# Kernel optimization log

Measured on AMD Instinct MI355X. Metric: run time of the kernel, lower is better.

## Reference

```python
import jax, jax.numpy as jnp
import numpy as np

N_NODES = 100000
N_EDGES = 3200000
IN_DIM = 512
OUT_DIM = 256


def setup_inputs() -> dict:
    key = jax.random.key(0)
    k1, k2, k3, k4, k5 = jax.random.split(key, 5)
    features = jax.random.normal(k1, (N_NODES, IN_DIM), dtype=jnp.float32)
    adj_rows = jax.random.randint(k2, (N_EDGES,), 0, N_NODES, dtype=jnp.int32)
    adj_cols = jax.random.randint(k3, (N_EDGES,), 0, N_NODES, dtype=jnp.int32)
    # normalized adjacency values (e.g., 1/sqrt(d_i d_j)); random positive here
    adj_vals = jax.random.uniform(k4, (N_EDGES,), dtype=jnp.float32) * (1.0 / 32.0)
    # xavier uniform for kernel
    limit = np.sqrt(6.0 / (IN_DIM + OUT_DIM)).astype(np.float32)
    kernel = jax.random.uniform(k5, (IN_DIM, OUT_DIM), dtype=jnp.float32, minval=-limit, maxval=limit)
    bias = jnp.zeros((OUT_DIM,), dtype=jnp.float32)
    skip_weight = jnp.ones((OUT_DIM,), dtype=jnp.float32)
    return {
        "features": features,
        "adj_rows": adj_rows,
        "adj_cols": adj_cols,
        "adj_vals": adj_vals,
        "kernel": kernel,
        "bias": bias,
        "skip_weight": skip_weight,
    }


def reference(features, adj_rows, adj_cols, adj_vals, kernel, bias, skip_weight):
    # dense feature transform: [N, in] @ [in, out] -> [N, out]
    xw = jnp.matmul(features, kernel)
    # SpMM: aggregate[i] = sum_e val[e] * xw[col[e]] over edges with row[e] == i
    msgs = adj_vals[:, None] * xw[adj_cols]            # [E, out] gather
    agg = jax.ops.segment_sum(msgs, adj_rows, num_segments=N_NODES)  # [N, out] scatter-add
    out = xw * skip_weight + agg + bias                # skip scale + bias epilogue
    return jax.nn.selu(out)
```

## Files before the change

### kernel.cpp

```cpp
#include <hip/hip_runtime.h>
#include <hip/hip_bf16.h>
#include <cstdint>
#include <cstddef>

#define IN_DIM 512
#define OUT_DIM 256
#define BROWS 128
#define NBUCK_MAX 1024
#define CAP 4608

typedef __bf16 bf16x8 __attribute__((ext_vector_type(8)));
typedef float f32x4 __attribute__((ext_vector_type(4)));

__device__ __forceinline__ unsigned short f2bf(float f) {
    __bf16 h = (__bf16)f;
    return __builtin_bit_cast(unsigned short, h);
}
__device__ __forceinline__ float bf2f(unsigned short u) {
    unsigned int x = ((unsigned int)u) << 16;
    return __builtin_bit_cast(float, x);
}
__device__ __forceinline__ float selu(float x) {
    const float kScale = 1.0507009873554805f;
    const float kAlpha = 1.6732632423543772f;
    return (x > 0.f) ? kScale * x : kScale * kAlpha * (expf(x) - 1.f);
}

__global__ void k_convW(const float* __restrict__ W, unsigned short* __restrict__ Wt) {
    int idx = blockIdx.x * 256 + threadIdx.x;
    int n = idx & (OUT_DIM - 1);
    int k = idx >> 8;
    if (k < IN_DIM) Wt[n * IN_DIM + k] = f2bf(W[k * OUT_DIM + n]);
}

__launch_bounds__(512, 2)
__global__ void k_gemm(const float* __restrict__ A, const unsigned short* __restrict__ Wt,
                       signed char* __restrict__ xq, float* __restrict__ scales, int M) {
    __shared__ unsigned short lA[128 * 32];
    __shared__ unsigned short lB[256 * 32];
    __shared__ float lrm[128];
    const int t = threadIdx.x;
    const int wave = t >> 6, lane = t & 63;
    const int wr = wave >> 2, wc = wave & 3;
    const int m0 = blockIdx.x * 128;
    const int mlo = lane & 15, kq = lane >> 4;

    if (t < 128) lrm[t] = 0.f;

    f32x4 acc[4][4] = {};

    for (int k0 = 0; k0 < IN_DIM; k0 += 32) {
        #pragma unroll
        for (int p = 0; p < 2; ++p) {
            int idx = p * 512 + t;
            int r = idx >> 3, c4 = idx & 7;
            int gr = m0 + r; if (gr >= M) gr = M - 1;
            const float4 v = *reinterpret_cast<const float4*>(&A[(size_t)gr * IN_DIM + k0 + c4 * 4]);
            ushort4 u;
            u.x = f2bf(v.x); u.y = f2bf(v.y); u.z = f2bf(v.z); u.w = f2bf(v.w);
            *reinterpret_cast<ushort4*>(&lA[r * 32 + c4 * 4]) = u;
        }
        #pragma unroll
        for (int p = 0; p < 2; ++p) {
            int idx = p * 512 + t;
            int n = idx >> 2, c8 = idx & 3;
            const uint4 v = *reinterpret_cast<const uint4*>(&Wt[(size_t)n * IN_DIM + k0 + c8 * 8]);
            *reinterpret_cast<uint4*>(&lB[n * 32 + c8 * 8]) = v;
        }
        __syncthreads();

        bf16x8 af[4], bfr[4];
        #pragma unroll
        for (int mt = 0; mt < 4; ++mt)
            af[mt] = *reinterpret_cast<const bf16x8*>(&lA[(wr * 64 + mt * 16 + mlo) * 32 + kq * 8]);
        #pragma unroll
        for (int nt = 0; nt < 4; ++nt)
            bfr[nt] = *reinterpret_cast<const bf16x8*>(&lB[(wc * 64 + nt * 16 + mlo) * 32 + kq * 8]);
        #pragma unroll
        for (int mt = 0; mt < 4; ++mt)
            #pragma unroll
            for (int nt = 0; nt < 4; ++nt)
                acc[mt][nt] = __builtin_amdgcn_mfma_f32_16x16x32_bf16(af[mt], bfr[nt], acc[mt][nt], 0, 0, 0);
        __syncthreads();
    }

    #pragma unroll
    for (int mt = 0; mt < 4; ++mt) {
        #pragma unroll
        for (int i = 0; i < 4; ++i) {
            float m = fmaxf(fmaxf(fabsf(acc[mt][0][i]), fabsf(acc[mt][1][i])),
                            fmaxf(fabsf(acc[mt][2][i]), fabsf(acc[mt][3][i])));
            m = fmaxf(m, __shfl_xor(m, 1));
            m = fmaxf(m, __shfl_xor(m, 2));
            m = fmaxf(m, __shfl_xor(m, 4));
            m = fmaxf(m, __shfl_xor(m, 8));
            if (mlo == 0)
                atomicMax(reinterpret_cast<int*>(&lrm[wr * 64 + mt * 16 + kq * 4 + i]),
                          __float_as_int(m));
        }
    }
    __syncthreads();

    #pragma unroll
    for (int mt = 0; mt < 4; ++mt) {
        #pragma unroll
        for (int i = 0; i < 4; ++i) {
            const int rl = wr * 64 + mt * 16 + kq * 4 + i;
            const int row = m0 + rl;
            const float rm = lrm[rl];
            const float inv = (rm > 0.f) ? (127.f / rm) : 0.f;
            if (row < M) {
                #pragma unroll
                for (int nt = 0; nt < 4; ++nt) {
                    int q = (int)rintf(acc[mt][nt][i] * inv);
                    xq[(size_t)row * OUT_DIM + wc * 64 + nt * 16 + mlo] = (signed char)q;
                }
            }
        }
    }
    if (t < 128) {
        int row = m0 + t;
        if (row < M) scales[row] = lrm[t] * (1.f / 127.f);
    }
}

__launch_bounds__(512)
__global__ void k_bhist(const int* __restrict__ rows, int* __restrict__ bcnt, int E) {
    __shared__ int cnt[NBUCK_MAX];
    const int t = threadIdx.x;
    const int base = blockIdx.x * 8192;
    cnt[t] = 0; cnt[t + 512] = 0;
    __syncthreads();
    #pragma unroll
    for (int p = 0; p < 4; ++p) {
        const int i = base + p * 2048 + (t << 2);
        if (i + 4 <= E) {
            int4 r4 = *reinterpret_cast<const int4*>(&rows[i]);
            atomicAdd(&cnt[r4.x >> 7], 1);
            atomicAdd(&cnt[r4.y >> 7], 1);
            atomicAdd(&cnt[r4.z >> 7], 1);
            atomicAdd(&cnt[r4.w >> 7], 1);
        } else if (i < E) {
            for (int j = i; j < E && j < i + 4; ++j) atomicAdd(&cnt[rows[j] >> 7], 1);
        }
    }
    __syncthreads();
    if (cnt[t] > 0) atomicAdd(&bcnt[t], cnt[t]);
    if (cnt[t + 512] > 0) atomicAdd(&bcnt[t + 512], cnt[t + 512]);
}

__launch_bounds__(NBUCK_MAX)
__global__ void k_bscan(const int* __restrict__ bcnt, int* __restrict__ bbase,
                        int* __restrict__ bcursor, int nbuck, int E) {
    const int t = threadIdx.x;
    __shared__ int sh[NBUCK_MAX];
    int v = (t < nbuck) ? bcnt[t] : 0;
    sh[t] = v;
    __syncthreads();
    for (int off = 1; off < NBUCK_MAX; off <<= 1) {
        int x = (t >= off) ? sh[t - off] : 0;
        __syncthreads();
        sh[t] += x;
        __syncthreads();
    }
    int ex = sh[t] - v;
    bbase[t] = ex;
    bcursor[t] = ex;
    if (t == 0) bbase[NBUCK_MAX] = E;
}

__launch_bounds__(512)
__global__ void k_bin(const int* __restrict__ rows, const int* __restrict__ cols,
                      const float* __restrict__ vals, const float* __restrict__ scales,
                      int* __restrict__ bcursor, int2* __restrict__ binned, int E) {
    __shared__ int cnt[NBUCK_MAX];
    __shared__ int scn[512];
    __shared__ int dlt[NBUCK_MAX];
    const int t = threadIdx.x;
    const int base = blockIdx.x * 8192;

    cnt[t] = 0; cnt[t + 512] = 0;
    __syncthreads();

    int er[16], ec[16];
    float ev[16];
    #pragma unroll
    for (int p = 0; p < 4; ++p) {
        const int i = base + p * 2048 + (t << 2);
        if (i + 4 <= E) {
            int4 r4 = *reinterpret_cast<const int4*>(&rows[i]);
            int4 c4 = *reinterpret_cast<const int4*>(&cols[i]);
            float4 v4 = *reinterpret_cast<const float4*>(&vals[i]);
            er[4*p+0] = r4.x; ec[4*p+0] = c4.x; ev[4*p+0] = v4.x * scales[c4.x];
            er[4*p+1] = r4.y; ec[4*p+1] = c4.y; ev[4*p+1] = v4.y * scales[c4.y];
            er[4*p+2] = r4.z; ec[4*p+2] = c4.z; ev[4*p+2] = v4.z * scales[c4.z];
            er[4*p+3] = r4.w; ec[4*p+3] = c4.w; ev[4*p+3] = v4.w * scales[c4.w];
        } else {
            #pragma unroll
            for (int j = 0; j < 4; ++j) {
                int idx = i + j;
                bool ok = idx < E;
                er[4*p+j] = ok ? rows[idx] : -1;
                ec[4*p+j] = ok ? cols[idx] : 0;
                ev[4*p+j] = ok ? vals[idx] * scales[cols[idx]] : 0.f;
            }
        }
    }

    #pragma unroll
    for (int k = 0; k < 16; ++k)
        if (er[k] >= 0) atomicAdd(&cnt[er[k] >> 7], 1);
    __syncthreads();

    int v0 = cnt[2 * t], v1 = cnt[2 * t + 1];
    int s = v0 + v1;
    scn[t] = s;
    __syncthreads();
    for (int off = 1; off < 512; off <<= 1) {
        int x = (t >= off) ? scn[t - off] : 0;
        __syncthreads();
        scn[t] += x;
        __syncthreads();
    }
    int exp_ = scn[t] - s;
    int ex0 = exp_, ex1 = exp_ + v0;

    int d0 = 0, d1 = 0;
    if (v0 > 0) d0 = atomicAdd(&bcursor[2 * t], v0) - ex0;
    if (v1 > 0) d1 = atomicAdd(&bcursor[2 * t + 1], v1) - ex1;
    dlt[2 * t] = d0; dlt[2 * t + 1] = d1;
    cnt[2 * t] = ex0; cnt[2 * t + 1] = ex1;
    __syncthreads();

    #pragma unroll
    for (int k = 0; k < 16; ++k) {
        if (er[k] >= 0) {
            int b = er[k] >> 7;
            int lp = atomicAdd(&cnt[b], 1);
            binned[(size_t)(dlt[b] + lp)] =
                make_int2(ec[k] | ((er[k] & 127) << 17), __float_as_int(ev[k]));
        }
    }
}

__launch_bounds__(512)
__global__ void k_aggb(const signed char* __restrict__ xq,
                       const float* __restrict__ scales,
                       const int2* __restrict__ binned,
                       const int* __restrict__ bbase,
                       const float* __restrict__ skipw,
                       const float* __restrict__ bias,
                       float* __restrict__ out, int M) {
    __shared__ int2 lrec[CAP];
    __shared__ int lrs[BROWS + 1];
    __shared__ int lcur[BROWS];
    const int b = blockIdx.x, t = threadIdx.x;
    const int wave = t >> 6, lane = t & 63;
    const int start = bbase[b], end = bbase[b + 1];
    const int cnt = end - start;
    const int d4 = lane * 4;

    if (cnt <= CAP) {
        if (t < BROWS) lcur[t] = 0;
        __syncthreads();
        for (int i = start + t; i < end; i += 512)
            atomicAdd(&lcur[binned[i].x >> 17], 1);
        __syncthreads();
        int v = 0;
        if (t < BROWS) { v = lcur[t]; lrs[t] = v; }
        __syncthreads();
        for (int off = 1; off < BROWS; off <<= 1) {
            int x = 0;
            if (t < BROWS && t >= off) x = lrs[t - off];
            __syncthreads();
            if (t < BROWS) lrs[t] += x;
            __syncthreads();
        }
        int ex = 0;
        if (t < BROWS) ex = lrs[t] - v;
        __syncthreads();
        if (t < BROWS) { lrs[t] = ex; lcur[t] = ex; }
        if (t == 0) lrs[BROWS] = cnt;
        __syncthreads();
        for (int i = start + t; i < end; i += 512) {
            int2 rec = binned[i];
            int pos = atomicAdd(&lcur[rec.x >> 17], 1);
            lrec[pos] = rec;
        }
        __syncthreads();
        for (int rr = 0; rr < BROWS / 8; ++rr) {
            const int r = wave * (BROWS / 8) + rr;
            const int grow = b * BROWS + r;
            if (grow >= M) continue;
            const int s = lrs[r], e = lrs[r + 1];
            float a0 = 0.f, a1 = 0.f, a2 = 0.f, a3 = 0.f;
            int p = s;
            for (; p + 8 <= e; p += 8) {
                int cs[8]; float vs[8];
                #pragma unroll
                for (int u = 0; u < 8; ++u) {
                    int2 c = lrec[p + u];
                    cs[u] = c.x & 0x1FFFF; vs[u] = __int_as_float(c.y);
                }
                int g[8];
                #pragma unroll
                for (int u = 0; u < 8; ++u)
                    g[u] = *reinterpret_cast<const int*>(&xq[(size_t)cs[u] * OUT_DIM + d4]);
                #pragma unroll
                for (int u = 0; u < 8; ++u) {
                    a0 += vs[u] * (float)(signed char)(g[u]);
                    a1 += vs[u] * (float)(signed char)(g[u] >> 8);
                    a2 += vs[u] * (float)(signed char)(g[u] >> 16);
                    a3 += vs[u] * (float)(g[u] >> 24);
                }
            }
            for (; p < e; ++p) {
                int2 c = lrec[p];
                float v2 = __int_as_float(c.y);
                int g = *reinterpret_cast<const int*>(&xq[(size_t)(c.x & 0x1FFFF) * OUT_DIM + d4]);
                a0 += v2 * (float)(signed char)(g);
                a1 += v2 * (float)(signed char)(g >> 8);
                a2 += v2 * (float)(signed char)(g >> 16);
                a3 += v2 * (float)(g >> 24);
            }
            int w = *reinterpret_cast<const int*>(&xq[(size_t)grow * OUT_DIM + d4]);
            float sc = scales[grow];
            float x0 = (float)(signed char)(w)        * sc;
            float x1 = (float)(signed char)(w >> 8)   * sc;
            float x2 = (float)(signed char)(w >> 16)  * sc;
            float x3 = (float)(w >> 24)               * sc;
            float4 sw = *reinterpret_cast<const float4*>(&skipw[d4]);
            float4 bi = *reinterpret_cast<const float4*>(&bias[d4]);
            float4 r4;
            r4.x = selu(a0 + x0 * sw.x + bi.x);
            r4.y = selu(a1 + x1 * sw.y + bi.y);
            r4.z = selu(a2 + x2 * sw.z + bi.z);
            r4.w = selu(a3 + x3 * sw.w + bi.w);
            *reinterpret_cast<float4*>(&out[(size_t)grow * OUT_DIM + d4]) = r4;
        }
    } else {
        for (int rr = 0; rr < BROWS / 8; ++rr) {
            const int r = wave * (BROWS / 8) + rr;
            const int grow = b * BROWS + r;
            if (grow >= M) continue;
            float a0 = 0.f, a1 = 0.f, a2 = 0.f, a3 = 0.f;
            for (int i = start; i < end; ++i) {
                int2 c = binned[i];
                if ((c.x >> 17) != r) continue;
                float v2 = __int_as_float(c.y);
                int g = *reinterpret_cast<const int*>(&xq[(size_t)(c.x & 0x1FFFF) * OUT_DIM + d4]);
                a0 += v2 * (float)(signed char)(g);
                a1 += v2 * (float)(signed char)(g >> 8);
                a2 += v2 * (float)(signed char)(g >> 16);
                a3 += v2 * (float)(g >> 24);
            }
            int w = *reinterpret_cast<const int*>(&xq[(size_t)grow * OUT_DIM + d4]);
            float sc = scales[grow];
            float x0 = (float)(signed char)(w)        * sc;
            float x1 = (float)(signed char)(w >> 8)   * sc;
            float x2 = (float)(signed char)(w >> 16)  * sc;
            float x3 = (float)(w >> 24)               * sc;
            float4 sw = *reinterpret_cast<const float4*>(&skipw[d4]);
            float4 bi = *reinterpret_cast<const float4*>(&bias[d4]);
            float4 r4;
            r4.x = selu(a0 + x0 * sw.x + bi.x);
            r4.y = selu(a1 + x1 * sw.y + bi.y);
            r4.z = selu(a2 + x2 * sw.z + bi.z);
            r4.w = selu(a3 + x3 * sw.w + bi.w);
            *reinterpret_cast<float4*>(&out[(size_t)grow * OUT_DIM + d4]) = r4;
        }
    }
}

__global__ void k_hist(const int* __restrict__ rows, int* __restrict__ counts, int E) {
    int i = (blockIdx.x * 256 + threadIdx.x) * 4;
    if (i + 4 <= E) {
        int4 r = *reinterpret_cast<const int4*>(&rows[i]);
        atomicAdd(&counts[r.x], 1);
        atomicAdd(&counts[r.y], 1);
        atomicAdd(&counts[r.z], 1);
        atomicAdd(&counts[r.w], 1);
    } else {
        for (int j = i; j < E; ++j) atomicAdd(&counts[rows[j]], 1);
    }
}

__global__ void k_scan1(const int* __restrict__ counts, int* __restrict__ rs,
                        int* __restrict__ bsum, int N) {
    int b = blockIdx.x, t = threadIdx.x;
    int base = b * 1024 + t * 4;
    int4 v = make_int4(0, 0, 0, 0);
    if (base + 4 <= N) v = *reinterpret_cast<const int4*>(&counts[base]);
    else {
        if (base + 0 < N) v.x = counts[base + 0];
        if (base + 1 < N) v.y = counts[base + 1];
        if (base + 2 < N) v.z = counts[base + 2];
        if (base + 3 < N) v.w = counts[base + 3];
    }
    int s0 = v.x, s1 = s0 + v.y, s2 = s1 + v.z, s3 = s2 + v.w;
    __shared__ int sh[256];
    sh[t] = s3; __syncthreads();
    for (int off = 1; off < 256; off <<= 1) {
        int x = (t >= off) ? sh[t - off] : 0;
        __syncthreads();
        sh[t] += x;
        __syncthreads();
    }
    int ex = sh[t] - s3;
    if (base + 0 < N) rs[base + 0] = ex;
    if (base + 1 < N) rs[base + 1] = ex + s0;
    if (base + 2 < N) rs[base + 2] = ex + s1;
    if (base + 3 < N) rs[base + 3] = ex + s2;
    if (t == 255) bsum[b] = sh[255];
}

__global__ void k_scan2(const int* __restrict__ bsum, int* __restrict__ boff, int nb) {
    int t = threadIdx.x;
    __shared__ int sh[256];
    int v = (t < nb) ? bsum[t] : 0;
    sh[t] = v; __syncthreads();
    for (int off = 1; off < 256; off <<= 1) {
        int x = (t >= off) ? sh[t - off] : 0;
        __syncthreads();
        sh[t] += x;
        __syncthreads();
    }
    if (t < nb) boff[t] = sh[t] - v;
}

__global__ void k_scan3(int* __restrict__ rs, int* __restrict__ cursor,
                        const int* __restrict__ boff, int N, int E) {
    int b = blockIdx.x, t = threadIdx.x;
    int base = b * 1024 + t * 4;
    int o = boff[b];
    #pragma unroll
    for (int j = 0; j < 4; ++j) {
        if (base + j < N) {
            int v = rs[base + j] + o;
            rs[base + j] = v;
            cursor[base + j] = v;
        }
    }
    if (b == 0 && t == 0) rs[N] = E;
}

__global__ void k_scatter(const int* __restrict__ rows, const int* __restrict__ cols,
                          const float* __restrict__ vals, const float* __restrict__ scales,
                          int* __restrict__ cursor, int2* __restrict__ ecv, int E) {
    int i = (blockIdx.x * 256 + threadIdx.x) * 4;
    if (i + 4 <= E) {
        int4 r = *reinterpret_cast<const int4*>(&rows[i]);
        int4 c = *reinterpret_cast<const int4*>(&cols[i]);
        float4 v = *reinterpret_cast<const float4*>(&vals[i]);
        int p0 = atomicAdd(&cursor[r.x], 1); ecv[p0] = make_int2(c.x, __float_as_int(v.x * scales[c.x]));
        int p1 = atomicAdd(&cursor[r.y], 1); ecv[p1] = make_int2(c.y, __float_as_int(v.y * scales[c.y]));
        int p2 = atomicAdd(&cursor[r.z], 1); ecv[p2] = make_int2(c.z, __float_as_int(v.z * scales[c.z]));
        int p3 = atomicAdd(&cursor[r.w], 1); ecv[p3] = make_int2(c.w, __float_as_int(v.w * scales[c.w]));
    } else {
        for (int j = i; j < E; ++j) {
            int p = atomicAdd(&cursor[rows[j]], 1);
            ecv[p] = make_int2(cols[j], __float_as_int(vals[j] * scales[cols[j]]));
        }
    }
}

__launch_bounds__(256)
__global__ void k_agg(const signed char* __restrict__ xq,
                      const float* __restrict__ scales,
                      const int2* __restrict__ ecv,
                      const int* __restrict__ rs,
                      const float* __restrict__ skipw,
                      const float* __restrict__ bias,
                      float* __restrict__ out, int M) {
    const int wave = threadIdx.x >> 6, lane = threadIdx.x & 63;
    const int node = blockIdx.x * 4 + wave;
    if (node >= M) return;
    const int s = __builtin_amdgcn_readfirstlane(rs[node]);
    const int e = __builtin_amdgcn_readfirstlane(rs[node + 1]);
    const int d4 = lane * 4;

    float a0 = 0.f, a1 = 0.f, a2 = 0.f, a3 = 0.f;
    int p = s;
    constexpr int U = 8;
    for (; p + U <= e; p += U) {
        int   cs[U];
        float vs[U];
        #pragma unroll
        for (int u = 0; u < U; ++u) {
            int2 c = ecv[p + u];
            cs[u] = c.x; vs[u] = __int_as_float(c.y);
        }
        int g[U];
        #pragma unroll
        for (int u = 0; u < U; ++u)
            g[u] = *reinterpret_cast<const int*>(&xq[(size_t)cs[u] * OUT_DIM + d4]);
        #pragma unroll
        for (int u = 0; u < U; ++u) {
            a0 += vs[u] * (float)(signed char)(g[u]);
            a1 += vs[u] * (float)(signed char)(g[u] >> 8);
            a2 += vs[u] * (float)(signed char)(g[u] >> 16);
            a3 += vs[u] * (float)(g[u] >> 24);
        }
    }
    for (; p < e; ++p) {
        int2 c = ecv[p];
        float v = __int_as_float(c.y);
        int g = *reinterpret_cast<const int*>(&xq[(size_t)c.x * OUT_DIM + d4]);
        a0 += v * (float)(signed char)(g);
        a1 += v * (float)(signed char)(g >> 8);
        a2 += v * (float)(signed char)(g >> 16);
        a3 += v * (float)(g >> 24);
    }

    int w = *reinterpret_cast<const int*>(&xq[(size_t)node * OUT_DIM + d4]);
    float sc = scales[node];
    float x0 = (float)(signed char)(w)        * sc;
    float x1 = (float)(signed char)(w >> 8)   * sc;
    float x2 = (float)(signed char)(w >> 16)  * sc;
    float x3 = (float)(w >> 24)               * sc;

    float4 sw = *reinterpret_cast<const float4*>(&skipw[d4]);
    float4 bi = *reinterpret_cast<const float4*>(&bias[d4]);
    float4 r;
    r.x = selu(a0 + x0 * sw.x + bi.x);
    r.y = selu(a1 + x1 * sw.y + bi.y);
    r.z = selu(a2 + x2 * sw.z + bi.z);
    r.w = selu(a3 + x3 * sw.w + bi.w);
    *reinterpret_cast<float4*>(&out[(size_t)node * OUT_DIM + d4]) = r;
}

extern "C" void kernel_launch(void* const* d_in, const int* in_sizes, int n_in,
                              void* d_out, int out_size, void* d_ws, size_t ws_size,
                              hipStream_t stream) {
    const float* features = (const float*)d_in[0];
    const int*   adj_rows = (const int*)d_in[1];
    const int*   adj_cols = (const int*)d_in[2];
    const float* adj_vals = (const float*)d_in[3];
    const float* Wk       = (const float*)d_in[4];
    const float* bias     = (const float*)d_in[5];
    const float* skipw    = (const float*)d_in[6];
    float* out = (float*)d_out;

    const int M = in_sizes[0] / IN_DIM;
    const int E = in_sizes[1];

    char* w = (char*)d_ws;
    size_t off = 0;
    auto carve = [&](size_t bytes) -> void* {
        void* p = w + off;
        off = (off + bytes + 255) & ~(size_t)255;
        return p;
    };
    signed char* xq = (signed char*)carve((size_t)M * OUT_DIM);
    float* scales   = (float*)carve((size_t)M * 4);
    unsigned short* Wt = (unsigned short*)carve((size_t)IN_DIM * OUT_DIM * 2);
    int*  counts = (int*)carve((size_t)M * 4);
    int*  rs     = (int*)carve((size_t)(M + 1) * 4);
    int*  cursor = (int*)carve((size_t)M * 4);
    int*  bsum   = (int*)carve(256 * 4);
    int*  boff   = (int*)carve(256 * 4);
    int*  bcnt   = (int*)carve((NBUCK_MAX + 1) * 4);
    int*  bbase  = (int*)carve((NBUCK_MAX + 1) * 4);
    int*  bcur   = (int*)carve((NBUCK_MAX + 1) * 4);
    int2* ecv    = (int2*)carve((size_t)E * 8);
    int2* binned = (int2*)carve((size_t)E * 8);
    const int nbuck = (M + BROWS - 1) / BROWS;
    const bool use_binned = (off <= ws_size) && (nbuck <= NBUCK_MAX) && (M <= (1 << 17));

    k_convW<<<(IN_DIM * OUT_DIM + 255) / 256, 256, 0, stream>>>(Wk, Wt);
    k_gemm<<<(M + 127) / 128, 512, 0, stream>>>(features, Wt, xq, scales, M);

    if (use_binned) {
        hipMemsetAsync(bcnt, 0, (NBUCK_MAX + 1) * 4, stream);
        k_bhist<<<(E + 8191) / 8192, 512, 0, stream>>>(adj_rows, bcnt, E);
        k_bscan<<<1, NBUCK_MAX, 0, stream>>>(bcnt, bbase, bcur, nbuck, E);
        k_bin<<<(E + 8191) / 8192, 512, 0, stream>>>(adj_rows, adj_cols, adj_vals, scales, bcur, binned, E);
        k_aggb<<<nbuck, 512, 0, stream>>>(xq, scales, binned, bbase, skipw, bias, out, M);
    } else {
        hipMemsetAsync(counts, 0, (size_t)M * 4, stream);
        k_hist<<<(E / 4 + 255) / 256, 256, 0, stream>>>(adj_rows, counts, E);
        int nb = (M + 1023) / 1024;
        k_scan1<<<nb, 256, 0, stream>>>(counts, rs, bsum, M);
        k_scan2<<<1, 256, 0, stream>>>(bsum, boff, nb);
        k_scan3<<<nb, 256, 0, stream>>>(rs, cursor, boff, M, E);
        k_scatter<<<(E / 4 + 255) / 256, 256, 0, stream>>>(adj_rows, adj_cols, adj_vals, scales, cursor, ecv, E);
        k_agg<<<(M + 3) / 4, 256, 0, stream>>>(xq, scales, ecv, rs, skipw, bias, out, M);
    }
}
```

Baseline: 556.5 us.

## Double-buffer GEMM LDS tiles and split binned records into row bytes

The GEMM now keeps two LDS buffers and prefetches the next K-slice into registers while MFMAs run on the current one, which halves the barriers per iteration. The binning stage now writes the local row index into a separate byte array next to the (col, val) pairs. The aggregation kernel counts rows by reading only those bytes, keeps them in registers, and reads each 8-byte record once during placement instead of twice. In exchange there is more LDS and register pressure in the GEMM and one extra small global stream.

```diff
diff --git a/kernel.cpp b/kernel.cpp
--- a/kernel.cpp
+++ b/kernel.cpp
@@ -8,6 +8,7 @@
 #define BROWS 128
 #define NBUCK_MAX 1024
 #define CAP 4608
+#define NJ 9
 
 typedef __bf16 bf16x8 __attribute__((ext_vector_type(8)));
 typedef float f32x4 __attribute__((ext_vector_type(4)));
@@ -36,8 +37,8 @@
 __launch_bounds__(512, 2)
 __global__ void k_gemm(const float* __restrict__ A, const unsigned short* __restrict__ Wt,
                        signed char* __restrict__ xq, float* __restrict__ scales, int M) {
-    __shared__ unsigned short lA[128 * 32];
-    __shared__ unsigned short lB[256 * 32];
+    __shared__ unsigned short lA[2][128 * 32];
+    __shared__ unsigned short lB[2][256 * 32];
     __shared__ float lrm[128];
     const int t = threadIdx.x;
     const int wave = t >> 6, lane = t & 63;
@@ -45,45 +46,64 @@
     const int m0 = blockIdx.x * 128;
     const int mlo = lane & 15, kq = lane >> 4;
 
+    const int ar0 = t >> 3,           ac0 = (t & 7) * 4;
+    const int ar1 = (512 + t) >> 3,   ac1 = ac0;
+    const int bn0 = t >> 2,           bc0 = (t & 3) * 8;
+    const int bn1 = (512 + t) >> 2,   bc1 = bc0;
+    int agr0 = m0 + ar0; if (agr0 >= M) agr0 = M - 1;
+    int agr1 = m0 + ar1; if (agr1 >= M) agr1 = M - 1;
+
     if (t < 128) lrm[t] = 0.f;
 
+    float4 pa0, pa1;
+    uint4  pb0, pb1;
+    auto LOAD = [&](int k0) {
+        pa0 = *reinterpret_cast<const float4*>(&A[(size_t)agr0 * IN_DIM + k0 + ac0]);
+        pa1 = *reinterpret_cast<const float4*>(&A[(size_t)agr1 * IN_DIM + k0 + ac1]);
+        pb0 = *reinterpret_cast<const uint4*>(&Wt[(size_t)bn0 * IN_DIM + k0 + bc0]);
+        pb1 = *reinterpret_cast<const uint4*>(&Wt[(size_t)bn1 * IN_DIM + k0 + bc1]);
+    };
+    auto STORE = [&](int buf) {
+        ushort4 u0, u1;
+        u0.x = f2bf(pa0.x); u0.y = f2bf(pa0.y); u0.z = f2bf(pa0.z); u0.w = f2bf(pa0.w);
+        u1.x = f2bf(pa1.x); u1.y = f2bf(pa1.y); u1.z = f2bf(pa1.z); u1.w = f2bf(pa1.w);
+        *reinterpret_cast<ushort4*>(&lA[buf][ar0 * 32 + ac0]) = u0;
+        *reinterpret_cast<ushort4*>(&lA[buf][ar1 * 32 + ac1]) = u1;
+        *reinterpret_cast<uint4*>(&lB[buf][bn0 * 32 + bc0]) = pb0;
+        *reinterpret_cast<uint4*>(&lB[buf][bn1 * 32 + bc1]) = pb1;
+    };
+
     f32x4 acc[4][4] = {};
 
-    for (int k0 = 0; k0 < IN_DIM; k0 += 32) {
-        #pragma unroll
-        for (int p = 0; p < 2; ++p) {
-            int idx = p * 512 + t;
-            int r = idx >> 3, c4 = idx & 7;
-            int gr = m0 + r; if (gr >= M) gr = M - 1;
-            const float4 v = *reinterpret_cast<const float4*>(&A[(size_t)gr * IN_DIM + k0 + c4 * 4]);
-            ushort4 u;
-            u.x = f2bf(v.x); u.y = f2bf(v.y); u.z = f2bf(v.z); u.w = f2bf(v.w);
-            *reinterpret_cast<ushort4*>(&lA[r * 32 + c4 * 4]) = u;
-        }
-        #pragma unroll
-        for (int p = 0; p < 2; ++p) {
-            int idx = p * 512 + t;
-            int n = idx >> 2, c8 = idx & 3;
-            const uint4 v = *reinterpret_cast<const uint4*>(&Wt[(size_t)n * IN_DIM + k0 + c8 * 8]);
-            *reinterpret_cast<uint4*>(&lB[n * 32 + c8 * 8]) = v;
-        }
-        __syncthreads();
+    LOAD(0);
+    STORE(0);
+    __syncthreads();
+
+    for (int k0 = 0, it = 0; k0 < IN_DIM; k0 += 32, ++it) {
+        const int buf = it & 1;
+        const bool more = (k0 + 32 < IN_DIM);
+        if (more) LOAD(k0 + 32);
 
         bf16x8 af[4], bfr[4];
         #pragma unroll
         for (int mt = 0; mt < 4; ++mt)
-            af[mt] = *reinterpret_cast<const bf16x8*>(&lA[(wr * 64 + mt * 16 + mlo) * 32 + kq * 8]);
+            af[mt] = *reinterpret_cast<const bf16x8*>(&lA[buf][(wr * 64 + mt * 16 + mlo) * 32 + kq * 8]);
         #pragma unroll
         for (int nt = 0; nt < 4; ++nt)
-            bfr[nt] = *reinterpret_cast<const bf16x8*>(&lB[(wc * 64 + nt * 16 + mlo) * 32 + kq * 8]);
+            bfr[nt] = *reinterpret_cast<const bf16x8*>(&lB[buf][(wc * 64 + nt * 16 + mlo) * 32 + kq * 8]);
         #pragma unroll
         for (int mt = 0; mt < 4; ++mt)
             #pragma unroll
             for (int nt = 0; nt < 4; ++nt)
                 acc[mt][nt] = __builtin_amdgcn_mfma_f32_16x16x32_bf16(af[mt], bfr[nt], acc[mt][nt], 0, 0, 0);
-        __syncthreads();
-    }
-
+
+        if (more) {
+            STORE(buf ^ 1);
+            __syncthreads();
+        }
+    }
+
+    __syncthreads();
     #pragma unroll
     for (int mt = 0; mt < 4; ++mt) {
         #pragma unroll
@@ -172,7 +192,8 @@
 __launch_bounds__(512)
 __global__ void k_bin(const int* __restrict__ rows, const int* __restrict__ cols,
                       const float* __restrict__ vals, const float* __restrict__ scales,
-                      int* __restrict__ bcursor, int2* __restrict__ binned, int E) {
+                      int* __restrict__ bcursor, int2* __restrict__ bcv,
+                      unsigned char* __restrict__ brow, int E) {
     __shared__ int cnt[NBUCK_MAX];
     __shared__ int scn[512];
     __shared__ int dlt[NBUCK_MAX];
@@ -237,8 +258,9 @@
         if (er[k] >= 0) {
             int b = er[k] >> 7;
             int lp = atomicAdd(&cnt[b], 1);
-            binned[(size_t)(dlt[b] + lp)] =
-                make_int2(ec[k] | ((er[k] & 127) << 17), __float_as_int(ev[k]));
+            int pos = dlt[b] + lp;
+            brow[pos] = (unsigned char)(er[k] & 127);
+            bcv[(size_t)pos] = make_int2(ec[k], __float_as_int(ev[k]));
         }
     }
 }
@@ -246,7 +268,8 @@
 __launch_bounds__(512)
 __global__ void k_aggb(const signed char* __restrict__ xq,
                        const float* __restrict__ scales,
-                       const int2* __restrict__ binned,
+                       const int2* __restrict__ bcv,
+                       const unsigned char* __restrict__ brow,
                        const int* __restrict__ bbase,
                        const float* __restrict__ skipw,
                        const float* __restrict__ bias,
@@ -263,8 +286,15 @@
     if (cnt <= CAP) {
         if (t < BROWS) lcur[t] = 0;
         __syncthreads();
-        for (int i = start + t; i < end; i += 512)
-            atomicAdd(&lcur[binned[i].x >> 17], 1);
+        unsigned char rr_[NJ];
+        #pragma unroll
+        for (int j = 0; j < NJ; ++j) {
+            int idx = start + j * 512 + t;
+            rr_[j] = (idx < end) ? brow[idx] : 255;
+        }
+        #pragma unroll
+        for (int j = 0; j < NJ; ++j)
+            if (rr_[j] != 255) atomicAdd(&lcur[rr_[j]], 1);
         __syncthreads();
         int v = 0;
         if (t < BROWS) { v = lcur[t]; lrs[t] = v; }
@@ -282,10 +312,13 @@
         if (t < BROWS) { lrs[t] = ex; lcur[t] = ex; }
         if (t == 0) lrs[BROWS] = cnt;
         __syncthreads();
-        for (int i = start + t; i < end; i += 512) {
-            int2 rec = binned[i];
-            int pos = atomicAdd(&lcur[rec.x >> 17], 1);
-            lrec[pos] = rec;
+        #pragma unroll
+        for (int j = 0; j < NJ; ++j) {
+            int idx = start + j * 512 + t;
+            if (idx < end) {
+                int pos = atomicAdd(&lcur[rr_[j]], 1);
+                lrec[pos] = bcv[idx];
+            }
         }
         __syncthreads();
         for (int rr = 0; rr < BROWS / 8; ++rr) {
@@ -300,7 +333,7 @@
                 #pragma unroll
                 for (int u = 0; u < 8; ++u) {
                     int2 c = lrec[p + u];
-                    cs[u] = c.x & 0x1FFFF; vs[u] = __int_as_float(c.y);
+                    cs[u] = c.x; vs[u] = __int_as_float(c.y);
                 }
                 int g[8];
                 #pragma unroll
@@ -317,7 +350,7 @@
             for (; p < e; ++p) {
                 int2 c = lrec[p];
                 float v2 = __int_as_float(c.y);
-                int g = *reinterpret_cast<const int*>(&xq[(size_t)(c.x & 0x1FFFF) * OUT_DIM + d4]);
+                int g = *reinterpret_cast<const int*>(&xq[(size_t)c.x * OUT_DIM + d4]);
                 a0 += v2 * (float)(signed char)(g);
                 a1 += v2 * (float)(signed char)(g >> 8);
                 a2 += v2 * (float)(signed char)(g >> 16);
@@ -345,10 +378,10 @@
             if (grow >= M) continue;
             float a0 = 0.f, a1 = 0.f, a2 = 0.f, a3 = 0.f;
             for (int i = start; i < end; ++i) {
-                int2 c = binned[i];
-                if ((c.x >> 17) != r) continue;
+                if (brow[i] != r) continue;
+                int2 c = bcv[i];
                 float v2 = __int_as_float(c.y);
-                int g = *reinterpret_cast<const int*>(&xq[(size_t)(c.x & 0x1FFFF) * OUT_DIM + d4]);
+                int g = *reinterpret_cast<const int*>(&xq[(size_t)c.x * OUT_DIM + d4]);
                 a0 += v2 * (float)(signed char)(g);
                 a1 += v2 * (float)(signed char)(g >> 8);
                 a2 += v2 * (float)(signed char)(g >> 16);
@@ -563,7 +596,8 @@
     int*  bbase  = (int*)carve((NBUCK_MAX + 1) * 4);
     int*  bcur   = (int*)carve((NBUCK_MAX + 1) * 4);
     int2* ecv    = (int2*)carve((size_t)E * 8);
-    int2* binned = (int2*)carve((size_t)E * 8);
+    int2* bcv    = (int2*)carve((size_t)E * 8);
+    unsigned char* brow = (unsigned char*)carve((size_t)E);
     const int nbuck = (M + BROWS - 1) / BROWS;
     const bool use_binned = (off <= ws_size) && (nbuck <= NBUCK_MAX) && (M <= (1 << 17));
 
@@ -574,8 +608,8 @@
         hipMemsetAsync(bcnt, 0, (NBUCK_MAX + 1) * 4, stream);
         k_bhist<<<(E + 8191) / 8192, 512, 0, stream>>>(adj_rows, bcnt, E);
         k_bscan<<<1, NBUCK_MAX, 0, stream>>>(bcnt, bbase, bcur, nbuck, E);
-        k_bin<<<(E + 8191) / 8192, 512, 0, stream>>>(adj_rows, adj_cols, adj_vals, scales, bcur, binned, E);
-        k_aggb<<<nbuck, 512, 0, stream>>>(xq, scales, binned, bbase, skipw, bias, out, M);
+        k_bin<<<(E + 8191) / 8192, 512, 0, stream>>>(adj_rows, adj_cols, adj_vals, scales, bcur, bcv, brow, E);
+        k_aggb<<<nbuck, 512, 0, stream>>>(xq, scales, bcv, brow, bbase, skipw, bias, out, M);
     } else {
         hipMemsetAsync(counts, 0, (size_t)M * 4, stream);
         k_hist<<<(E / 4 + 255) / 256, 256, 0, stream>>>(adj_rows, counts, E);
```

Measured after the change: 571.2 us. 2.6% more time.
